# Performance work log

Measured on AMD Instinct MI355X. Metric: run time of the kernel, lower is better.

## Reference

```python
import jax, jax.numpy as jnp
import numpy as np

B, S, D, H, DH, RANK = 1, 2048, 1024, 16, 64, 16
NUM_ITERS = 5
EPS = 1e-6


def setup_inputs() -> dict:
    ks = jax.random.split(jax.random.key(0), 8)
    scale = 1.0 / np.sqrt(D)
    return {
        "x": jax.random.normal(ks[0], (B, S, D), dtype=jnp.float32),
        "Wq": jax.random.normal(ks[1], (D, D), dtype=jnp.float32) * scale,
        "Wk": jax.random.normal(ks[2], (D, D), dtype=jnp.float32) * scale,
        "Wv": jax.random.normal(ks[3], (D, D), dtype=jnp.float32) * scale,
        "Wo": jax.random.normal(ks[4], (D, D), dtype=jnp.float32) * scale,
        "bandwidth": jnp.array(1.0, dtype=jnp.float32),
        "diag_scale": jnp.ones((1, H, 1), dtype=jnp.float32),
        "pos_embedding": jax.random.normal(ks[5], (2048, RANK), dtype=jnp.float32) * 0.02,
        "head_proj": jax.random.normal(ks[6], (H, RANK, RANK), dtype=jnp.float32) * 0.02,
        "reg": jnp.array(0.1, dtype=jnp.float32),
        "lambda_reg": jnp.array(0.1, dtype=jnp.float32),
    }


def reference(x, Wq, Wk, Wv, Wo, bandwidth, diag_scale, pos_embedding, head_proj, reg, lambda_reg):
    b, s, d = x.shape
    h, dh = H, DH

    def heads(t):  # (b,s,d) -> (b,h,s,dh)
        return t.reshape(b, s, h, dh).transpose(0, 2, 1, 3)

    q = heads(x @ Wq)
    k = heads(x @ Wk)
    v = heads(x @ Wv)

    # RBF kernel via norm trick: ||q-k||^2 = ||q||^2 + ||k||^2 - 2 q.k
    bw = jax.nn.softplus(bandwidth) + EPS
    q_nsq = jnp.sum(q * q, axis=-1, keepdims=True)            # (b,h,s,1)
    k_nsq = jnp.sum(k * k, axis=-1, keepdims=True)            # (b,h,s,1)
    dist_sq = q_nsq + jnp.swapaxes(k_nsq, -2, -1) - 2.0 * jnp.einsum('bhsd,bhtd->bhst', q, k)
    dist_sq = jnp.maximum(dist_sq, 0.0)
    K = jnp.exp(-dist_sq / (2.0 * bw * bw))                   # (b,h,s,s)

    lam = jax.nn.softplus(lambda_reg)

    # Preconditioner P = diag(d) + U U^T
    kdiag = jnp.diagonal(K, axis1=-2, axis2=-1)               # (b,h,s)
    diag_p = jax.nn.softplus(kdiag) * diag_scale + reg        # (b,h,s)
    U = jnp.einsum('sr,hrp->hsp', pos_embedding[:s], head_proj)  # (h,s,rank)

    # Preconditioned Richardson iteration for (K + lam I) alpha = V
    alpha = jnp.zeros_like(v)
    for _ in range(NUM_ITERS):
        r = v - (jnp.einsum('bhst,bhtd->bhsd', K, alpha) + lam * alpha)
        ut_r = jnp.einsum('htr,bhtd->bhrd', U, r)
        p = r * diag_p[..., None] + jnp.einsum('hsr,bhrd->bhsd', U, ut_r)
        alpha = alpha + p

    out = jnp.einsum('bhst,bhtd->bhsd', K, alpha)             # output = K alpha
    out = out.transpose(0, 2, 1, 3).reshape(b, s, d) @ Wo
    return out
```

## Files before the change

kernel.cpp:

```cpp
#include <hip/hip_runtime.h>
#include <cstdint>
#include <cstddef>

constexpr int kS  = 2048;
constexpr int kD  = 1024;
constexpr int kH  = 16;
constexpr int kDH = 64;
constexpr int kR  = 16;

typedef __attribute__((ext_vector_type(8))) short bf16x8;
typedef __attribute__((ext_vector_type(4))) float f32x4;

__device__ __forceinline__ unsigned short kar_f2bf(float x) {
  unsigned u = __float_as_uint(x);
  return (unsigned short)((u + 0x7FFFu + ((u >> 16) & 1u)) >> 16);
}
__device__ __forceinline__ float kar_bf2f(short h) {
  return __uint_as_float((unsigned)(unsigned short)h << 16);
}
__device__ __forceinline__ void kar_split_bf(float x, short& hi, short& lo) {
  unsigned short h = kar_f2bf(x);
  float hf = __uint_as_float((unsigned)h << 16);
  hi = (short)h;
  lo = (short)kar_f2bf(x - hf);
}

__global__ __launch_bounds__(64) void kar_scalars_kernel(const float* __restrict__ bw,
                                                         const float* __restrict__ lreg,
                                                         double* __restrict__ SC) {
  if (threadIdx.x == 0) {
    double b = log1p(exp((double)bw[0])) + 1e-6;
    SC[0] = 1.0 / (2.0 * b * b);
    SC[1] = log1p(exp((double)lreg[0]));
  }
}

__global__ __launch_bounds__(256) void kar_u_kernel(const float* __restrict__ pe,
                                                    const float* __restrict__ hp,
                                                    float* __restrict__ U) {
  int o = blockIdx.x * 256 + threadIdx.x;
  int r = o & 15, s = (o >> 4) & 2047, h = o >> 15;
  double acc = 0.0;
#pragma unroll
  for (int rp = 0; rp < kR; rp++)
    acc += (double)pe[s * kR + rp] * (double)hp[((h * kR) + rp) * kR + r];
  U[o] = (float)acc;
}

__global__ __launch_bounds__(256) void kar_utr_partial_kernel(
    const float* __restrict__ Ubuf, const float* __restrict__ rbuf,
    double* __restrict__ utrp) {
  const int h  = blockIdx.y;
  const int sb = blockIdx.x * 128;
  const int t  = threadIdx.x;
  __shared__ float Uch[32][16];
  __shared__ float Rch[32][64];
  double acc[4] = {};
  for (int cs = 0; cs < 128; cs += 32) {
    __syncthreads();
    if (t < 128) {
      const int i = t >> 2, f = (t & 3) * 4;
      *(float4*)&Uch[i][f] = *(const float4*)&Ubuf[((size_t)(h * kS) + sb + cs + i) * kR + f];
    }
#pragma unroll
    for (int rep = 0; rep < 2; rep++) {
      const int e = t + rep * 256;
      const int i = e >> 4, c = (e & 15) * 4;
      *(float4*)&Rch[i][c] = *(const float4*)&rbuf[((size_t)(h * kS) + sb + cs + i) * kDH + c];
    }
    __syncthreads();
    for (int i = 0; i < 32; i++) {
#pragma unroll
      for (int rep = 0; rep < 4; rep++) {
        const int p = t + rep * 256;
        const int r = p >> 6, d = p & 63;
        acc[rep] += (double)Uch[i][r] * (double)Rch[i][d];
      }
    }
  }
#pragma unroll
  for (int rep = 0; rep < 4; rep++) {
    const int p = t + rep * 256;
    const int r = p >> 6, d = p & 63;
    utrp[(((size_t)(h * 16) + blockIdx.x) * kR + r) * kDH + d] = acc[rep];
  }
}

__global__ __launch_bounds__(256) void kar_utr_reduce_kernel(const double* __restrict__ utrp,
                                                             double* __restrict__ utr) {
  int o = blockIdx.x * 256 + threadIdx.x;
  int h = o >> 10, rd = o & 1023;
  double s = 0.0;
#pragma unroll
  for (int j = 0; j < 16; j++) s += utrp[(size_t)h * 16384 + (size_t)j * 1024 + rd];
  utr[o] = s;
}

__global__ __launch_bounds__(256) void kar_update_kernel(
    const float* __restrict__ rsrc, const double* __restrict__ dgp,
    const float* __restrict__ Ubuf, const double* __restrict__ utr,
    float* __restrict__ alpha, int first) {
  int e = blockIdx.x * 256 + threadIdx.x;
  const int d = e & 63;
  const int s = (e >> 6) & 2047;
  const int h = e >> 17;
  const double rv = (double)rsrc[e];
  const double dp = dgp[h * kS + s];
  const float*  Us = &Ubuf[((size_t)(h * kS) + s) * kR];
  const double* uh = &utr[(size_t)h * kR * kDH];
  double sum = 0.0;
#pragma unroll
  for (int ri = 0; ri < kR; ri++) sum += (double)Us[ri] * uh[ri * kDH + d];
  const double p = rv * dp + sum;
  const double an = (first ? 0.0 : (double)alpha[e]) + p;
  alpha[e] = (float)an;
}

__global__ __launch_bounds__(256) void kar_update_t_kernel(
    const float* __restrict__ rsrc, const double* __restrict__ dgp,
    const float* __restrict__ Ubuf, const double* __restrict__ utr,
    float* __restrict__ alpha, short* __restrict__ ath, short* __restrict__ atl,
    int first) {
  const int h = blockIdx.y, s0 = blockIdx.x * 64;
  __shared__ float T[64][65];
  const int t = threadIdx.x;
  const int r16 = t >> 4, c4 = (t & 15) * 4;
  const double* uh = &utr[(size_t)h * kR * kDH];
#pragma unroll
  for (int it = 0; it < 4; it++) {
    const int row = it * 16 + r16;
    const int s = s0 + row;
    const size_t eg = ((size_t)h * kS + s) * kDH + c4;
    const float4 rv4 = *(const float4*)&rsrc[eg];
    const double dp = dgp[h * kS + s];
    const float* Us = &Ubuf[((size_t)h * kS + s) * kR];
    double sum0 = 0.0, sum1 = 0.0, sum2 = 0.0, sum3 = 0.0;
#pragma unroll
    for (int ri = 0; ri < kR; ri++) {
      const double u = (double)Us[ri];
      const double* ur = &uh[ri * kDH + c4];
      sum0 += u * ur[0]; sum1 += u * ur[1];
      sum2 += u * ur[2]; sum3 += u * ur[3];
    }
    double a0 = (first ? 0.0 : (double)alpha[eg + 0]) + ((double)rv4.x * dp + sum0);
    double a1 = (first ? 0.0 : (double)alpha[eg + 1]) + ((double)rv4.y * dp + sum1);
    double a2 = (first ? 0.0 : (double)alpha[eg + 2]) + ((double)rv4.z * dp + sum2);
    double a3 = (first ? 0.0 : (double)alpha[eg + 3]) + ((double)rv4.w * dp + sum3);
    float4 o;
    o.x = (float)a0; o.y = (float)a1; o.z = (float)a2; o.w = (float)a3;
    *(float4*)&alpha[eg] = o;
    T[row][c4] = o.x; T[row][c4 + 1] = o.y; T[row][c4 + 2] = o.z; T[row][c4 + 3] = o.w;
  }
  __syncthreads();
#pragma unroll
  for (int it = 0; it < 4; it++) {
    int d = it * 16 + r16;
    float v0 = T[c4][d], v1 = T[c4 + 1][d], v2 = T[c4 + 2][d], v3 = T[c4 + 3][d];
    short h0, l0, h1, l1, h2, l2, h3, l3;
    kar_split_bf(v0, h0, l0); kar_split_bf(v1, h1, l1);
    kar_split_bf(v2, h2, l2); kar_split_bf(v3, h3, l3);
    *(short4*)&ath[((size_t)h * kDH + d) * kS + s0 + c4] = make_short4(h0, h1, h2, h3);
    *(short4*)&atl[((size_t)h * kDH + d) * kS + s0 + c4] = make_short4(l0, l1, l2, l3);
  }
}


__global__ __launch_bounds__(256) void kar_xsplit_kernel(const float* __restrict__ x,
                                                         short* __restrict__ xh,
                                                         short* __restrict__ xl) {
  size_t e = ((size_t)blockIdx.x * 256 + threadIdx.x) * 4;
  float4 a = *(const float4*)&x[e];
  short h0, l0, h1, l1, h2, l2, h3, l3;
  kar_split_bf(a.x, h0, l0); kar_split_bf(a.y, h1, l1);
  kar_split_bf(a.z, h2, l2); kar_split_bf(a.w, h3, l3);
  *(short4*)&xh[e] = make_short4(h0, h1, h2, h3);
  *(short4*)&xl[e] = make_short4(l0, l1, l2, l3);
}

__global__ __launch_bounds__(256) void kar_wsplit_kernel(
    const float* __restrict__ Wq, const float* __restrict__ Wk,
    const float* __restrict__ Wv, const float* __restrict__ Wo,
    short* __restrict__ WTh, short* __restrict__ WTl) {
  const float* W = (blockIdx.z == 0) ? Wq : (blockIdx.z == 1) ? Wk
                 : (blockIdx.z == 2) ? Wv : Wo;
  short* oh = WTh + (size_t)blockIdx.z * kD * kD;
  short* ol = WTl + (size_t)blockIdx.z * kD * kD;
  const int n0 = blockIdx.x * 64, k0 = blockIdx.y * 64;
  __shared__ float T[64][65];
  const int t = threadIdx.x;
  const int r16 = t >> 4, c4 = (t & 15) * 4;
#pragma unroll
  for (int it = 0; it < 4; it++) {
    int r = it * 16 + r16;
    float4 a = *(const float4*)&W[(size_t)(k0 + r) * kD + n0 + c4];
    T[r][c4] = a.x; T[r][c4 + 1] = a.y; T[r][c4 + 2] = a.z; T[r][c4 + 3] = a.w;
  }
  __syncthreads();
#pragma unroll
  for (int it = 0; it < 4; it++) {
    int n = it * 16 + r16;
    float v0 = T[c4][n], v1 = T[c4 + 1][n], v2 = T[c4 + 2][n], v3 = T[c4 + 3][n];
    short h0, l0, h1, l1, h2, l2, h3, l3;
    kar_split_bf(v0, h0, l0); kar_split_bf(v1, h1, l1);
    kar_split_bf(v2, h2, l2); kar_split_bf(v3, h3, l3);
    *(short4*)&oh[(size_t)(n0 + n) * kD + k0 + c4] = make_short4(h0, h1, h2, h3);
    *(short4*)&ol[(size_t)(n0 + n) * kD + k0 + c4] = make_short4(l0, l1, l2, l3);
  }
}

__global__ __launch_bounds__(256) void kar_mfma_gemm_qkv_kernel(
    const short* __restrict__ xh, const short* __restrict__ xl,
    const short* __restrict__ WTh, const short* __restrict__ WTl,
    float* __restrict__ v,
    short* __restrict__ qsh, short* __restrict__ qsl,
    short* __restrict__ ksh, short* __restrict__ ksl) {
  const int z = blockIdx.z;
  const short* Bh = WTh + (size_t)z * kD * kD;
  const short* Bl = WTl + (size_t)z * kD * kD;
  const int n0 = blockIdx.x * 64;
  const int m0 = blockIdx.y * 128;
  constexpr int LW = 40;
  __shared__ short Xh[128 * LW], Xl[128 * LW], Wh[64 * LW], Wl[64 * LW];
  const int t = threadIdx.x, lane = t & 63, wv = t >> 6;
  const int wm = wv >> 1, wn = wv & 1, l16 = lane & 15, qd = lane >> 4;
  f32x4 acc[4][2];
#pragma unroll
  for (int i = 0; i < 4; i++)
#pragma unroll
    for (int j = 0; j < 2; j++) acc[i][j] = (f32x4){0.f, 0.f, 0.f, 0.f};
  const int xrow = t >> 1, xc = (t & 1) * 16;
  for (int k0 = 0; k0 < kD; k0 += 32) {
    __syncthreads();
    {
      const size_t xs = (size_t)(m0 + xrow) * kD + k0 + xc;
      *(bf16x8*)&Xh[xrow * LW + xc]     = *(const bf16x8*)&xh[xs];
      *(bf16x8*)&Xh[xrow * LW + xc + 8] = *(const bf16x8*)&xh[xs + 8];
      *(bf16x8*)&Xl[xrow * LW + xc]     = *(const bf16x8*)&xl[xs];
      *(bf16x8*)&Xl[xrow * LW + xc + 8] = *(const bf16x8*)&xl[xs + 8];
    }
    if (t < 128) {
      const int wrow = t >> 1, wc = (t & 1) * 16;
      const size_t wsrc = (size_t)(n0 + wrow) * kD + k0 + wc;
      *(bf16x8*)&Wh[wrow * LW + wc]     = *(const bf16x8*)&Bh[wsrc];
      *(bf16x8*)&Wh[wrow * LW + wc + 8] = *(const bf16x8*)&Bh[wsrc + 8];
    } else {
      const int t2 = t - 128, wrow = t2 >> 1, wc = (t2 & 1) * 16;
      const size_t wsrc = (size_t)(n0 + wrow) * kD + k0 + wc;
      *(bf16x8*)&Wl[wrow * LW + wc]     = *(const bf16x8*)&Bl[wsrc];
      *(bf16x8*)&Wl[wrow * LW + wc + 8] = *(const bf16x8*)&Bl[wsrc + 8];
    }
    __syncthreads();
    bf16x8 bH[2], bL[2];
#pragma unroll
    for (int ni = 0; ni < 2; ni++) {
      const int rn = wn * 32 + ni * 16 + l16;
      bH[ni] = *(const bf16x8*)&Wh[rn * LW + qd * 8];
      bL[ni] = *(const bf16x8*)&Wl[rn * LW + qd * 8];
    }
#pragma unroll
    for (int mi = 0; mi < 4; mi++) {
      const int rm = wm * 64 + mi * 16 + l16;
      const bf16x8 aH = *(const bf16x8*)&Xh[rm * LW + qd * 8];
      const bf16x8 aL = *(const bf16x8*)&Xl[rm * LW + qd * 8];
#pragma unroll
      for (int ni = 0; ni < 2; ni++) {
        acc[mi][ni] = __builtin_amdgcn_mfma_f32_16x16x32_bf16(aH, bH[ni], acc[mi][ni], 0, 0, 0);
        acc[mi][ni] = __builtin_amdgcn_mfma_f32_16x16x32_bf16(aL, bH[ni], acc[mi][ni], 0, 0, 0);
        acc[mi][ni] = __builtin_amdgcn_mfma_f32_16x16x32_bf16(aH, bL[ni], acc[mi][ni], 0, 0, 0);
      }
    }
  }
  const int h = blockIdx.x;
#pragma unroll
  for (int mi = 0; mi < 4; mi++)
#pragma unroll
    for (int ni = 0; ni < 2; ni++) {
      const int d = wn * 32 + ni * 16 + l16;
#pragma unroll
      for (int r = 0; r < 4; r++) {
        const int s = m0 + wm * 64 + mi * 16 + qd * 4 + r;
        const float val = acc[mi][ni][r];
        const size_t idx = (((size_t)h * kS) + s) * kDH + d;
        if (z == 2) {
          v[idx] = val;
        } else {
          short hh, ll; kar_split_bf(val, hh, ll);
          if (z == 0) { qsh[idx] = hh; qsl[idx] = ll; }
          else        { ksh[idx] = hh; ksl[idx] = ll; }
        }
      }
    }
}

__global__ __launch_bounds__(256) void kar_mfma_gemm_wo_kernel(
    const short* __restrict__ th, const short* __restrict__ tl,
    const short* __restrict__ Bh, const short* __restrict__ Bl,
    float* __restrict__ outp) {
  const int n0 = blockIdx.x * 64;
  const int m0 = blockIdx.y * 128;
  constexpr int LW = 40;
  __shared__ short Xh[128 * LW], Xl[128 * LW], Wh[64 * LW], Wl[64 * LW];
  const int t = threadIdx.x, lane = t & 63, wv = t >> 6;
  const int wm = wv >> 1, wn = wv & 1, l16 = lane & 15, qd = lane >> 4;
  f32x4 acc[4][2];
#pragma unroll
  for (int i = 0; i < 4; i++)
#pragma unroll
    for (int j = 0; j < 2; j++) acc[i][j] = (f32x4){0.f, 0.f, 0.f, 0.f};
  const int xrow = t >> 1, xc = (t & 1) * 16;
  for (int k0 = 0; k0 < kD; k0 += 32) {
    __syncthreads();
    {
      const size_t xs = (size_t)(m0 + xrow) * kD + k0 + xc;
      *(bf16x8*)&Xh[xrow * LW + xc]     = *(const bf16x8*)&th[xs];
      *(bf16x8*)&Xh[xrow * LW + xc + 8] = *(const bf16x8*)&th[xs + 8];
      *(bf16x8*)&Xl[xrow * LW + xc]     = *(const bf16x8*)&tl[xs];
      *(bf16x8*)&Xl[xrow * LW + xc + 8] = *(const bf16x8*)&tl[xs + 8];
    }
    if (t < 128) {
      const int wrow = t >> 1, wc = (t & 1) * 16;
      const size_t wsrc = (size_t)(n0 + wrow) * kD + k0 + wc;
      *(bf16x8*)&Wh[wrow * LW + wc]     = *(const bf16x8*)&Bh[wsrc];
      *(bf16x8*)&Wh[wrow * LW + wc + 8] = *(const bf16x8*)&Bh[wsrc + 8];
    } else {
      const int t2 = t - 128, wrow = t2 >> 1, wc = (t2 & 1) * 16;
      const size_t wsrc = (size_t)(n0 + wrow) * kD + k0 + wc;
      *(bf16x8*)&Wl[wrow * LW + wc]     = *(const bf16x8*)&Bl[wsrc];
      *(bf16x8*)&Wl[wrow * LW + wc + 8] = *(const bf16x8*)&Bl[wsrc + 8];
    }
    __syncthreads();
    bf16x8 bH[2], bL[2];
#pragma unroll
    for (int ni = 0; ni < 2; ni++) {
      const int rn = wn * 32 + ni * 16 + l16;
      bH[ni] = *(const bf16x8*)&Wh[rn * LW + qd * 8];
      bL[ni] = *(const bf16x8*)&Wl[rn * LW + qd * 8];
    }
#pragma unroll
    for (int mi = 0; mi < 4; mi++) {
      const int rm = wm * 64 + mi * 16 + l16;
      const bf16x8 aH = *(const bf16x8*)&Xh[rm * LW + qd * 8];
      const bf16x8 aL = *(const bf16x8*)&Xl[rm * LW + qd * 8];
#pragma unroll
      for (int ni = 0; ni < 2; ni++) {
        acc[mi][ni] = __builtin_amdgcn_mfma_f32_16x16x32_bf16(aH, bH[ni], acc[mi][ni], 0, 0, 0);
        acc[mi][ni] = __builtin_amdgcn_mfma_f32_16x16x32_bf16(aL, bH[ni], acc[mi][ni], 0, 0, 0);
        acc[mi][ni] = __builtin_amdgcn_mfma_f32_16x16x32_bf16(aH, bL[ni], acc[mi][ni], 0, 0, 0);
      }
    }
  }
#pragma unroll
  for (int mi = 0; mi < 4; mi++)
#pragma unroll
    for (int ni = 0; ni < 2; ni++) {
      const int col = n0 + wn * 32 + ni * 16 + l16;
#pragma unroll
      for (int r = 0; r < 4; r++) {
        const int s = m0 + wm * 64 + mi * 16 + qd * 4 + r;
        outp[(size_t)s * kD + col] = acc[mi][ni][r];
      }
    }
}

__global__ __launch_bounds__(256) void kar_norms2_kernel(
    const short* __restrict__ qsh, const short* __restrict__ qsl,
    const short* __restrict__ ksh, const short* __restrict__ ksl,
    double* __restrict__ qn, double* __restrict__ kn) {
  int o = blockIdx.x * 256 + threadIdx.x;
  const short *sh, *sl; double* dst; int p;
  if (o < kH * kS) { sh = qsh; sl = qsl; dst = qn; p = o; }
  else             { sh = ksh; sl = ksl; dst = kn; p = o - kH * kS; }
  const short* rh = sh + (size_t)p * kDH;
  const short* rl = sl + (size_t)p * kDH;
  double s = 0.0;
  for (int i = 0; i < kDH; i += 4) {
    short4 a = *(const short4*)&rh[i];
    short4 b = *(const short4*)&rl[i];
    double e0 = (double)kar_bf2f(a.x) + (double)kar_bf2f(b.x);
    double e1 = (double)kar_bf2f(a.y) + (double)kar_bf2f(b.y);
    double e2 = (double)kar_bf2f(a.z) + (double)kar_bf2f(b.z);
    double e3 = (double)kar_bf2f(a.w) + (double)kar_bf2f(b.w);
    s += e0 * e0 + e1 * e1 + e2 * e2 + e3 * e3;
  }
  dst[p] = s;
}

__global__ __launch_bounds__(256) void kar_diagp2_kernel(
    const short* __restrict__ qsh, const short* __restrict__ qsl,
    const short* __restrict__ ksh, const short* __restrict__ ksl,
    const double* __restrict__ qn, const double* __restrict__ kn,
    const double* __restrict__ SC, const float* __restrict__ dsc,
    const float* __restrict__ reg, double* __restrict__ dgp) {
  int o = blockIdx.x * 256 + threadIdx.x;
  int h = o >> 11;
  const short* qh = qsh + (size_t)o * kDH;
  const short* ql = qsl + (size_t)o * kDH;
  const short* kh = ksh + (size_t)o * kDH;
  const short* kl = ksl + (size_t)o * kDH;
  double dot = 0.0;
  for (int i = 0; i < kDH; i++) {
    double qi = (double)kar_bf2f(qh[i]) + (double)kar_bf2f(ql[i]);
    double ki = (double)kar_bf2f(kh[i]) + (double)kar_bf2f(kl[i]);
    dot += qi * ki;
  }
  double dist = fmax(qn[o] + kn[o] - 2.0 * dot, 0.0);
  double Kss = exp(-dist * SC[0]);
  double sp  = log1p(exp(Kss));
  dgp[o] = sp * (double)dsc[h] + (double)reg[0];
}

template <bool FINAL>
__global__ __launch_bounds__(256, 2) void kar_mfma_iter4_kernel(
    const short* __restrict__ qsh, const short* __restrict__ qsl,
    const short* __restrict__ ksh, const short* __restrict__ ksl,
    const short* __restrict__ ath, const short* __restrict__ atl,
    const float* __restrict__ alpha, const float* __restrict__ v,
    const double* __restrict__ qn, const double* __restrict__ kn,
    const double* __restrict__ SC, float* __restrict__ outp,
    short* __restrict__ tmph, short* __restrict__ tmpl) {
  constexpr int LDW = 72;
  __shared__ short Kh[64 * LDW], Kl[64 * LDW];
  __shared__ short Ah[64 * LDW], Al[64 * LDW];
  __shared__ short Ph[64 * LDW];
  __shared__ float qns[64];
  const int h   = blockIdx.y;
  const int s0  = blockIdx.x * 64;
  const int tid = threadIdx.x;
  const int lane = tid & 63;
  const int wv   = tid >> 6;
  const int l16  = lane & 15;
  const int qd   = lane >> 4;
  const int row = tid >> 2, c8 = (tid & 3) * 16;
  bf16x8 qH[4][2], qL[4][2];
#pragma unroll
  for (int sq = 0; sq < 4; sq++) {
    const size_t qb = (((size_t)h * kS) + s0 + sq * 16 + l16) * kDH;
    qH[sq][0] = *(const bf16x8*)&qsh[qb + qd * 8];
    qH[sq][1] = *(const bf16x8*)&qsh[qb + 32 + qd * 8];
    qL[sq][0] = *(const bf16x8*)&qsl[qb + qd * 8];
    qL[sq][1] = *(const bf16x8*)&qsl[qb + 32 + qd * 8];
  }
  if (tid < 64) qns[tid] = (float)qn[h * kS + s0 + tid];
  const float cc = (float)SC[0];
  f32x4 acco[4];
#pragma unroll
  for (int i = 0; i < 4; i++) acco[i] = (f32x4){0.f, 0.f, 0.f, 0.f};

  for (int t0 = 0; t0 < kS; t0 += 64) {
    __syncthreads();
    {
      const size_t ksrc = (((size_t)h * kS) + t0 + row) * kDH;
      *(bf16x8*)&Kh[row * LDW + c8]     = *(const bf16x8*)&ksh[ksrc + c8];
      *(bf16x8*)&Kh[row * LDW + c8 + 8] = *(const bf16x8*)&ksh[ksrc + c8 + 8];
      *(bf16x8*)&Kl[row * LDW + c8]     = *(const bf16x8*)&ksl[ksrc + c8];
      *(bf16x8*)&Kl[row * LDW + c8 + 8] = *(const bf16x8*)&ksl[ksrc + c8 + 8];
      const size_t asrc = ((size_t)h * kDH + row) * kS + t0;
      *(bf16x8*)&Ah[row * LDW + c8]     = *(const bf16x8*)&ath[asrc + c8];
      *(bf16x8*)&Ah[row * LDW + c8 + 8] = *(const bf16x8*)&ath[asrc + c8 + 8];
      *(bf16x8*)&Al[row * LDW + c8]     = *(const bf16x8*)&atl[asrc + c8];
      *(bf16x8*)&Al[row * LDW + c8 + 8] = *(const bf16x8*)&atl[asrc + c8 + 8];
    }
    const float knr = (float)kn[h * kS + t0 + wv * 16 + l16];
    __syncthreads();
    f32x4 accp[4];
#pragma unroll
    for (int i = 0; i < 4; i++) accp[i] = (f32x4){0.f, 0.f, 0.f, 0.f};
#pragma unroll
    for (int kt = 0; kt < 2; kt++) {
      const int ko = kt * 32 + qd * 8;
      const bf16x8 bH = *(const bf16x8*)&Kh[(wv * 16 + l16) * LDW + ko];
      const bf16x8 bL = *(const bf16x8*)&Kl[(wv * 16 + l16) * LDW + ko];
#pragma unroll
      for (int sq = 0; sq < 4; sq++) {
        accp[sq] = __builtin_amdgcn_mfma_f32_16x16x32_bf16(qH[sq][kt], bH, accp[sq], 0, 0, 0);
        accp[sq] = __builtin_amdgcn_mfma_f32_16x16x32_bf16(qL[sq][kt], bH, accp[sq], 0, 0, 0);
        accp[sq] = __builtin_amdgcn_mfma_f32_16x16x32_bf16(qH[sq][kt], bL, accp[sq], 0, 0, 0);
      }
    }
#pragma unroll
    for (int sq = 0; sq < 4; sq++) {
#pragma unroll
      for (int r = 0; r < 4; r++) {
        const int srow = sq * 16 + qd * 4 + r;
        const float e2 = fmaf(2.0f, accp[sq][r], -(qns[srow] + knr));
        const float val = __expf(fminf(e2, 0.0f) * cc);
        Ph[srow * LDW + wv * 16 + l16] = (short)kar_f2bf(val);
      }
    }
    __syncthreads();
#pragma unroll
    for (int kt = 0; kt < 2; kt++) {
      const int ko = kt * 32 + qd * 8;
      const bf16x8 bH = *(const bf16x8*)&Ah[(wv * 16 + l16) * LDW + ko];
      const bf16x8 bL = *(const bf16x8*)&Al[(wv * 16 + l16) * LDW + ko];
#pragma unroll
      for (int sq = 0; sq < 4; sq++) {
        const bf16x8 pH = *(const bf16x8*)&Ph[(sq * 16 + l16) * LDW + ko];
        acco[sq] = __builtin_amdgcn_mfma_f32_16x16x32_bf16(pH, bH, acco[sq], 0, 0, 0);
        acco[sq] = __builtin_amdgcn_mfma_f32_16x16x32_bf16(pH, bL, acco[sq], 0, 0, 0);
      }
    }
  }
  const int d = wv * 16 + l16;
  if (FINAL) {
#pragma unroll
    for (int sq = 0; sq < 4; sq++) {
#pragma unroll
      for (int r = 0; r < 4; r++) {
        const int s = s0 + sq * 16 + qd * 4 + r;
        short hh, ll; kar_split_bf(acco[sq][r], hh, ll);
        tmph[(size_t)s * kD + h * kDH + d] = hh;
        tmpl[(size_t)s * kD + h * kDH + d] = ll;
      }
    }
  } else {
    const float lamf = (float)SC[1];
#pragma unroll
    for (int sq = 0; sq < 4; sq++) {
#pragma unroll
      for (int r = 0; r < 4; r++) {
        const int s = s0 + sq * 16 + qd * 4 + r;
        const size_t eg = ((size_t)h * kS + s) * kDH + d;
        outp[eg] = v[eg] - (acco[sq][r] + lamf * alpha[eg]);
      }
    }
  }
}

__global__ __launch_bounds__(256) void kar_gemm_qkv_f32_kernel(
    const float* __restrict__ x,
    const float* __restrict__ Wq, const float* __restrict__ Wk, const float* __restrict__ Wv,
    float* __restrict__ q, float* __restrict__ k, float* __restrict__ v) {
  const float* W = (blockIdx.z == 0) ? Wq : (blockIdx.z == 1) ? Wk : Wv;
  float* outp    = (blockIdx.z == 0) ? q  : (blockIdx.z == 1) ? k  : v;
  const int n0 = blockIdx.x * 64;
  const int m0 = blockIdx.y * 64;
  const int tid = threadIdx.x;
  const int tx = tid & 15, ty = tid >> 4;
  __shared__ float As[16][68];
  __shared__ float Bs[16][68];
  double acc[4][4] = {};
  const int lr = tid >> 2;
  const int lk = (tid & 3) * 4;
  const int br = tid >> 4;
  const int bc = (tid & 15) * 4;
  for (int k0 = 0; k0 < kD; k0 += 16) {
    const float4 a4 = *(const float4*)&x[(size_t)(m0 + lr) * kD + k0 + lk];
    const float4 b4 = *(const float4*)&W[(size_t)(k0 + br) * kD + n0 + bc];
    __syncthreads();
    As[lk + 0][lr] = a4.x; As[lk + 1][lr] = a4.y;
    As[lk + 2][lr] = a4.z; As[lk + 3][lr] = a4.w;
    *(float4*)&Bs[br][bc] = b4;
    __syncthreads();
    float c32[4][4] = {};
#pragma unroll
    for (int kk = 0; kk < 16; kk++) {
      const float4 av = *(const float4*)&As[kk][ty * 4];
      const float4 bv = *(const float4*)&Bs[kk][tx * 4];
      const float a_[4] = {av.x, av.y, av.z, av.w};
      const float b_[4] = {bv.x, bv.y, bv.z, bv.w};
#pragma unroll
      for (int i = 0; i < 4; i++)
#pragma unroll
        for (int j = 0; j < 4; j++) c32[i][j] = fmaf(a_[i], b_[j], c32[i][j]);
    }
#pragma unroll
    for (int i = 0; i < 4; i++)
#pragma unroll
      for (int j = 0; j < 4; j++) acc[i][j] += (double)c32[i][j];
  }
  const int h = n0 >> 6;
#pragma unroll
  for (int i = 0; i < 4; i++) {
    const int s = m0 + ty * 4 + i;
    float4 o;
    o.x = (float)acc[i][0]; o.y = (float)acc[i][1];
    o.z = (float)acc[i][2]; o.w = (float)acc[i][3];
    *(float4*)&outp[((size_t)h * kS + s) * kDH + tx * 4] = o;
  }
}

__global__ __launch_bounds__(256) void kar_gemm_plain_kernel(
    const float* __restrict__ A, const float* __restrict__ W, float* __restrict__ C) {
  const int n0 = blockIdx.x * 64;
  const int m0 = blockIdx.y * 64;
  const int tid = threadIdx.x;
  const int tx = tid & 15, ty = tid >> 4;
  __shared__ float As[16][68];
  __shared__ float Bs[16][68];
  double acc[4][4] = {};
  const int lr = tid >> 2;
  const int lk = (tid & 3) * 4;
  const int br = tid >> 4;
  const int bc = (tid & 15) * 4;
  for (int k0 = 0; k0 < kD; k0 += 16) {
    const float4 a4 = *(const float4*)&A[(size_t)(m0 + lr) * kD + k0 + lk];
    const float4 b4 = *(const float4*)&W[(size_t)(k0 + br) * kD + n0 + bc];
    __syncthreads();
    As[lk + 0][lr] = a4.x; As[lk + 1][lr] = a4.y;
    As[lk + 2][lr] = a4.z; As[lk + 3][lr] = a4.w;
    *(float4*)&Bs[br][bc] = b4;
    __syncthreads();
    float c32[4][4] = {};
#pragma unroll
    for (int kk = 0; kk < 16; kk++) {
      const float4 av = *(const float4*)&As[kk][ty * 4];
      const float4 bv = *(const float4*)&Bs[kk][tx * 4];
      const float a_[4] = {av.x, av.y, av.z, av.w};
      const float b_[4] = {bv.x, bv.y, bv.z, bv.w};
#pragma unroll
      for (int i = 0; i < 4; i++)
#pragma unroll
        for (int j = 0; j < 4; j++) c32[i][j] = fmaf(a_[i], b_[j], c32[i][j]);
    }
#pragma unroll
    for (int i = 0; i < 4; i++)
#pragma unroll
      for (int j = 0; j < 4; j++) acc[i][j] += (double)c32[i][j];
  }
#pragma unroll
  for (int i = 0; i < 4; i++) {
    const int s = m0 + ty * 4 + i;
    float4 o;
    o.x = (float)acc[i][0]; o.y = (float)acc[i][1];
    o.z = (float)acc[i][2]; o.w = (float)acc[i][3];
    *(float4*)&C[(size_t)s * kD + n0 + tx * 4] = o;
  }
}

__global__ __launch_bounds__(256) void kar_norms_f32_kernel(const float* __restrict__ q,
                                                            const float* __restrict__ k,
                                                            double* __restrict__ qn,
                                                            double* __restrict__ kn) {
  int o = blockIdx.x * 256 + threadIdx.x;
  const float* src; double* dst; int p;
  if (o < kH * kS) { src = q; dst = qn; p = o; }
  else             { src = k; dst = kn; p = o - kH * kS; }
  const float* rowp = src + (size_t)p * kDH;
  double s = 0.0;
  for (int i = 0; i < kDH; i += 4) {
    float4 x4 = *(const float4*)&rowp[i];
    s += (double)x4.x * (double)x4.x + (double)x4.y * (double)x4.y +
         (double)x4.z * (double)x4.z + (double)x4.w * (double)x4.w;
  }
  dst[p] = s;
}

__global__ __launch_bounds__(256) void kar_diagp_f32_kernel(
    const float* __restrict__ q, const float* __restrict__ k,
    const double* __restrict__ qn, const double* __restrict__ kn,
    const double* __restrict__ SC, const float* __restrict__ dsc,
    const float* __restrict__ reg, double* __restrict__ dgp) {
  int o = blockIdx.x * 256 + threadIdx.x;
  int h = o >> 11;
  const float* qp = q + (size_t)o * kDH;
  const float* kp = k + (size_t)o * kDH;
  double dot = 0.0;
  for (int i = 0; i < kDH; i++) dot += (double)qp[i] * (double)kp[i];
  double dist = fmax(qn[o] + kn[o] - 2.0 * dot, 0.0);
  double Kss = exp(-dist * SC[0]);
  double sp  = log1p(exp(Kss));
  dgp[o] = sp * (double)dsc[h] + (double)reg[0];
}

template <bool FINAL>
__global__ __launch_bounds__(256, 2) void kar_mfma_iterA_kernel(
    const float* __restrict__ q, const float* __restrict__ k,
    const float* __restrict__ alpha, const float* __restrict__ v,
    const double* __restrict__ qn, const double* __restrict__ kn,
    const double* __restrict__ SC, float* __restrict__ outp) {
  constexpr int LDW = 72;
  __shared__ short Qh[64 * LDW], Ql[64 * LDW];
  __shared__ short Kh[64 * LDW], Kl[64 * LDW];
  __shared__ short Ph[64 * LDW], Pl[64 * LDW];
  __shared__ short Ah[64 * LDW], Al[64 * LDW];
  __shared__ float qns[64], kns[64];
  const int h   = blockIdx.y;
  const int s0  = blockIdx.x * 64;
  const int tid = threadIdx.x;
  const int lane = tid & 63;
  const int wv   = tid >> 6;
  const int l16  = lane & 15;
  const int qd   = lane >> 4;
  const int m16  = wv * 16;
  const float* qh = q + ((size_t)h * kS + s0) * kDH;
  const float* kh = k + (size_t)h * kS * kDH;
  const float* ah = alpha + (size_t)h * kS * kDH;
  {
    const int row = tid >> 4;
    const int c4  = (tid & 15) * 4;
#pragma unroll
    for (int rep = 0; rep < 4; rep++) {
      const int r = rep * 16 + row;
      const float4 a = *(const float4*)&qh[(size_t)r * kDH + c4];
      short h0, l0, h1, l1, h2, l2, h3, l3;
      kar_split_bf(a.x, h0, l0); kar_split_bf(a.y, h1, l1);
      kar_split_bf(a.z, h2, l2); kar_split_bf(a.w, h3, l3);
      *(short4*)&Qh[r * LDW + c4] = make_short4(h0, h1, h2, h3);
      *(short4*)&Ql[r * LDW + c4] = make_short4(l0, l1, l2, l3);
    }
    if (tid < 64) qns[tid] = (float)qn[h * kS + s0 + tid];
  }
  const float cc = (float)SC[0];
  f32x4 acco[4];
#pragma unroll
  for (int i = 0; i < 4; i++) acco[i] = (f32x4){0.f, 0.f, 0.f, 0.f};
  for (int t0 = 0; t0 < kS; t0 += 64) {
    __syncthreads();
    {
      const int row = tid >> 4;
      const int c4  = (tid & 15) * 4;
#pragma unroll
      for (int rep = 0; rep < 4; rep++) {
        const int r = rep * 16 + row;
        const float4 b = *(const float4*)&kh[(size_t)(t0 + r) * kDH + c4];
        short h0, l0, h1, l1, h2, l2, h3, l3;
        kar_split_bf(b.x, h0, l0); kar_split_bf(b.y, h1, l1);
        kar_split_bf(b.z, h2, l2); kar_split_bf(b.w, h3, l3);
        *(short4*)&Kh[r * LDW + c4] = make_short4(h0, h1, h2, h3);
        *(short4*)&Kl[r * LDW + c4] = make_short4(l0, l1, l2, l3);
        const float4 av = *(const float4*)&ah[(size_t)(t0 + r) * kDH + c4];
        kar_split_bf(av.x, h0, l0); kar_split_bf(av.y, h1, l1);
        kar_split_bf(av.z, h2, l2); kar_split_bf(av.w, h3, l3);
        Ah[(c4 + 0) * LDW + r] = h0; Al[(c4 + 0) * LDW + r] = l0;
        Ah[(c4 + 1) * LDW + r] = h1; Al[(c4 + 1) * LDW + r] = l1;
        Ah[(c4 + 2) * LDW + r] = h2; Al[(c4 + 2) * LDW + r] = l2;
        Ah[(c4 + 3) * LDW + r] = h3; Al[(c4 + 3) * LDW + r] = l3;
      }
      if (tid < 64) kns[tid] = (float)kn[h * kS + t0 + tid];
    }
    __syncthreads();
    f32x4 accp[4];
#pragma unroll
    for (int i = 0; i < 4; i++) accp[i] = (f32x4){0.f, 0.f, 0.f, 0.f};
#pragma unroll
    for (int kt = 0; kt < 2; kt++) {
      const int ko = kt * 32 + qd * 8;
      const bf16x8 aH = *(const bf16x8*)&Qh[(m16 + l16) * LDW + ko];
      const bf16x8 aL = *(const bf16x8*)&Ql[(m16 + l16) * LDW + ko];
#pragma unroll
      for (int nt = 0; nt < 4; nt++) {
        const bf16x8 bH = *(const bf16x8*)&Kh[(nt * 16 + l16) * LDW + ko];
        const bf16x8 bL = *(const bf16x8*)&Kl[(nt * 16 + l16) * LDW + ko];
        accp[nt] = __builtin_amdgcn_mfma_f32_16x16x32_bf16(aH, bH, accp[nt], 0, 0, 0);
        accp[nt] = __builtin_amdgcn_mfma_f32_16x16x32_bf16(aL, bH, accp[nt], 0, 0, 0);
        accp[nt] = __builtin_amdgcn_mfma_f32_16x16x32_bf16(aH, bL, accp[nt], 0, 0, 0);
      }
    }
#pragma unroll
    for (int nt = 0; nt < 4; nt++) {
      const int tcol = nt * 16 + l16;
      const float kv = kns[tcol];
#pragma unroll
      for (int r = 0; r < 4; r++) {
        const int srow = m16 + qd * 4 + r;
        const float e2 = fmaf(2.0f, accp[nt][r], -(qns[srow] + kv));
        const float val = __expf(fminf(e2, 0.0f) * cc);
        short hb, lb; kar_split_bf(val, hb, lb);
        Ph[srow * LDW + tcol] = hb;
        Pl[srow * LDW + tcol] = lb;
      }
    }
#pragma unroll
    for (int kt = 0; kt < 2; kt++) {
      const int ko = kt * 32 + qd * 8;
      const bf16x8 pH = *(const bf16x8*)&Ph[(m16 + l16) * LDW + ko];
      const bf16x8 pL = *(const bf16x8*)&Pl[(m16 + l16) * LDW + ko];
#pragma unroll
      for (int dt = 0; dt < 4; dt++) {
        const bf16x8 bH = *(const bf16x8*)&Ah[(dt * 16 + l16) * LDW + ko];
        const bf16x8 bL = *(const bf16x8*)&Al[(dt * 16 + l16) * LDW + ko];
        acco[dt] = __builtin_amdgcn_mfma_f32_16x16x32_bf16(pH, bH, acco[dt], 0, 0, 0);
        acco[dt] = __builtin_amdgcn_mfma_f32_16x16x32_bf16(pL, bH, acco[dt], 0, 0, 0);
        acco[dt] = __builtin_amdgcn_mfma_f32_16x16x32_bf16(pH, bL, acco[dt], 0, 0, 0);
      }
    }
  }
  if (FINAL) {
#pragma unroll
    for (int dt = 0; dt < 4; dt++) {
#pragma unroll
      for (int r = 0; r < 4; r++) {
        const int s = s0 + m16 + qd * 4 + r;
        const int d = dt * 16 + l16;
        outp[(size_t)s * kD + h * kDH + d] = acco[dt][r];
      }
    }
  } else {
    const float lamf = (float)SC[1];
#pragma unroll
    for (int dt = 0; dt < 4; dt++) {
#pragma unroll
      for (int r = 0; r < 4; r++) {
        const int s = s0 + m16 + qd * 4 + r;
        const int d = dt * 16 + l16;
        const size_t eg = ((size_t)h * kS + s) * kDH + d;
        outp[eg] = v[eg] - (acco[dt][r] + lamf * alpha[eg]);
      }
    }
  }
}

extern "C" void kernel_launch(void* const* d_in, const int* in_sizes, int n_in,
                              void* d_out, int out_size, void* d_ws, size_t ws_size,
                              hipStream_t stream) {
  (void)in_sizes; (void)n_in; (void)out_size;
  const float* x    = (const float*)d_in[0];
  const float* Wq   = (const float*)d_in[1];
  const float* Wk   = (const float*)d_in[2];
  const float* Wv   = (const float*)d_in[3];
  const float* Wo   = (const float*)d_in[4];
  const float* bw   = (const float*)d_in[5];
  const float* dsc  = (const float*)d_in[6];
  const float* pe   = (const float*)d_in[7];
  const float* hp   = (const float*)d_in[8];
  const float* reg  = (const float*)d_in[9];
  const float* lreg = (const float*)d_in[10];
  float* out = (float*)d_out;

  char* w = (char*)d_ws;
  size_t off = 0;
  auto take = [&](size_t bytes) -> void* {
    void* p = w + off;
    off += (bytes + 255) & ~(size_t)255;
    return p;
  };
  const size_t HSD = (size_t)kH * kS * kDH;

  float*  v_    = (float*)take(HSD * 4);
  float*  alpha = (float*)take(HSD * 4);
  float*  rbuf  = (float*)take(HSD * 4);
  short*  qsh   = (short*)take(HSD * 2);
  short*  qsl   = (short*)take(HSD * 2);
  short*  ksh   = (short*)take(HSD * 2);
  short*  ksl   = (short*)take(HSD * 2);
  short*  ath   = (short*)take(HSD * 2);
  short*  atl   = (short*)take(HSD * 2);
  short*  xh    = (short*)take((size_t)kS * kD * 2);
  short*  xl    = (short*)take((size_t)kS * kD * 2);
  short*  WTh   = (short*)take((size_t)4 * kD * kD * 2);
  short*  WTl   = (short*)take((size_t)4 * kD * kD * 2);
  double* qn    = (double*)take((size_t)kH * kS * 8);
  double* kn    = (double*)take((size_t)kH * kS * 8);
  double* dgp   = (double*)take((size_t)kH * kS * 8);
  float*  U     = (float*)take((size_t)kH * kS * kR * 4);
  double* utr   = (double*)take((size_t)kH * kR * kDH * 8);
  double* utrp  = (double*)take((size_t)kH * 16 * kR * kDH * 8);
  double* SC    = (double*)take(256);
  const size_t need_new = off;

  if (ws_size >= need_new) {
    kar_scalars_kernel<<<1, 64, 0, stream>>>(bw, lreg, SC);
    kar_xsplit_kernel<<<2048, 256, 0, stream>>>(x, xh, xl);
    kar_wsplit_kernel<<<dim3(16, 16, 4), 256, 0, stream>>>(Wq, Wk, Wv, Wo, WTh, WTl);
    kar_mfma_gemm_qkv_kernel<<<dim3(16, 16, 3), 256, 0, stream>>>(
        xh, xl, WTh, WTl, v_, qsh, qsl, ksh, ksl);
    kar_norms2_kernel<<<256, 256, 0, stream>>>(qsh, qsl, ksh, ksl, qn, kn);
    kar_u_kernel<<<2048, 256, 0, stream>>>(pe, hp, U);
    kar_diagp2_kernel<<<128, 256, 0, stream>>>(qsh, qsl, ksh, ksl, qn, kn, SC, dsc, reg, dgp);

    kar_utr_partial_kernel<<<dim3(16, kH), 256, 0, stream>>>(U, v_, utrp);
    kar_utr_reduce_kernel<<<64, 256, 0, stream>>>(utrp, utr);
    kar_update_t_kernel<<<dim3(32, kH), 256, 0, stream>>>(v_, dgp, U, utr, alpha, ath, atl, 1);

    for (int it = 1; it < 5; it++) {
      kar_mfma_iter4_kernel<false><<<dim3(32, kH), 256, 0, stream>>>(
          qsh, qsl, ksh, ksl, ath, atl, alpha, v_, qn, kn, SC, rbuf, nullptr, nullptr);
      kar_utr_partial_kernel<<<dim3(16, kH), 256, 0, stream>>>(U, rbuf, utrp);
      kar_utr_reduce_kernel<<<64, 256, 0, stream>>>(utrp, utr);
      kar_update_t_kernel<<<dim3(32, kH), 256, 0, stream>>>(rbuf, dgp, U, utr, alpha, ath, atl, 0);
    }

    kar_mfma_iter4_kernel<true><<<dim3(32, kH), 256, 0, stream>>>(
        qsh, qsl, ksh, ksl, ath, atl, alpha, v_, qn, kn, SC, rbuf, xh, xl);
    kar_mfma_gemm_wo_kernel<<<dim3(16, 16), 256, 0, stream>>>(
        xh, xl, WTh + (size_t)3 * kD * kD, WTl + (size_t)3 * kD * kD, out);
  } else {
    size_t off2 = 0;
    auto take2 = [&](size_t bytes) -> void* {
      void* p = w + off2;
      off2 += (bytes + 255) & ~(size_t)255;
      return p;
    };
    float*  q2    = (float*)take2(HSD * 4);
    float*  k2    = (float*)take2(HSD * 4);
    float*  v2    = (float*)take2(HSD * 4);
    float*  al2   = (float*)take2(HSD * 4);
    float*  rb2   = (float*)take2(HSD * 4);
    float*  tmp2  = (float*)take2((size_t)kS * kD * 4);
    double* qn2   = (double*)take2((size_t)kH * kS * 8);
    double* kn2   = (double*)take2((size_t)kH * kS * 8);
    double* dgp2  = (double*)take2((size_t)kH * kS * 8);
    float*  U2    = (float*)take2((size_t)kH * kS * kR * 4);
    double* utr2  = (double*)take2((size_t)kH * kR * kDH * 8);
    double* utrp2 = (double*)take2((size_t)kH * 16 * kR * kDH * 8);
    double* SC2   = (double*)take2(256);

    kar_scalars_kernel<<<1, 64, 0, stream>>>(bw, lreg, SC2);
    kar_gemm_qkv_f32_kernel<<<dim3(16, 32, 3), 256, 0, stream>>>(x, Wq, Wk, Wv, q2, k2, v2);
    kar_norms_f32_kernel<<<256, 256, 0, stream>>>(q2, k2, qn2, kn2);
    kar_u_kernel<<<2048, 256, 0, stream>>>(pe, hp, U2);
    kar_diagp_f32_kernel<<<128, 256, 0, stream>>>(q2, k2, qn2, kn2, SC2, dsc, reg, dgp2);

    kar_utr_partial_kernel<<<dim3(16, kH), 256, 0, stream>>>(U2, v2, utrp2);
    kar_utr_reduce_kernel<<<64, 256, 0, stream>>>(utrp2, utr2);
    kar_update_kernel<<<8192, 256, 0, stream>>>(v2, dgp2, U2, utr2, al2, 1);

    for (int it = 1; it < 5; it++) {
      kar_mfma_iterA_kernel<false><<<dim3(32, kH), 256, 0, stream>>>(
          q2, k2, al2, v2, qn2, kn2, SC2, rb2);
      kar_utr_partial_kernel<<<dim3(16, kH), 256, 0, stream>>>(U2, rb2, utrp2);
      kar_utr_reduce_kernel<<<64, 256, 0, stream>>>(utrp2, utr2);
      kar_update_kernel<<<8192, 256, 0, stream>>>(rb2, dgp2, U2, utr2, al2, 0);
    }
    kar_mfma_iterA_kernel<true><<<dim3(32, kH), 256, 0, stream>>>(
        q2, k2, al2, v2, qn2, kn2, SC2, tmp2);
    kar_gemm_plain_kernel<<<dim3(16, 32), 256, 0, stream>>>(tmp2, Wo, out);
  }
}
```

Baseline: 693.5 us.

## Fuse U^T r partial reduction into residual kernel and drop alpha low bf16 part

The residual kernel now computes the per-block U^T r partial sums in its epilogue, so the separate utr_partial launch inside the iteration loop is gone. The partial buffer is resized to 32 blocks per head to match. Alpha is also kept only as a single bf16 (hi) part, which halves the MFMA count and LDS/global traffic for the K*alpha product. The cost is lower precision in K*alpha, which could hurt accuracy of the Richardson iteration.

```diff
diff --git a/kernel.cpp b/kernel.cpp
--- a/kernel.cpp
+++ b/kernel.cpp
@@ -51,12 +51,12 @@
     const float* __restrict__ Ubuf, const float* __restrict__ rbuf,
     double* __restrict__ utrp) {
   const int h  = blockIdx.y;
-  const int sb = blockIdx.x * 128;
+  const int sb = blockIdx.x * 64;
   const int t  = threadIdx.x;
   __shared__ float Uch[32][16];
   __shared__ float Rch[32][64];
   double acc[4] = {};
-  for (int cs = 0; cs < 128; cs += 32) {
+  for (int cs = 0; cs < 64; cs += 32) {
     __syncthreads();
     if (t < 128) {
       const int i = t >> 2, f = (t & 3) * 4;
@@ -82,7 +82,7 @@
   for (int rep = 0; rep < 4; rep++) {
     const int p = t + rep * 256;
     const int r = p >> 6, d = p & 63;
-    utrp[(((size_t)(h * 16) + blockIdx.x) * kR + r) * kDH + d] = acc[rep];
+    utrp[(((size_t)(h * 32) + blockIdx.x) * kR + r) * kDH + d] = acc[rep];
   }
 }
 
@@ -92,7 +92,7 @@
   int h = o >> 10, rd = o & 1023;
   double s = 0.0;
 #pragma unroll
-  for (int j = 0; j < 16; j++) s += utrp[(size_t)h * 16384 + (size_t)j * 1024 + rd];
+  for (int j = 0; j < 32; j++) s += utrp[(size_t)h * 32768 + (size_t)j * 1024 + rd];
   utr[o] = s;
 }
 
@@ -119,8 +119,7 @@
 __global__ __launch_bounds__(256) void kar_update_t_kernel(
     const float* __restrict__ rsrc, const double* __restrict__ dgp,
     const float* __restrict__ Ubuf, const double* __restrict__ utr,
-    float* __restrict__ alpha, short* __restrict__ ath, short* __restrict__ atl,
-    int first) {
+    float* __restrict__ alpha, short* __restrict__ ath, int first) {
   const int h = blockIdx.y, s0 = blockIdx.x * 64;
   __shared__ float T[64][65];
   const int t = threadIdx.x;
@@ -156,11 +155,9 @@
   for (int it = 0; it < 4; it++) {
     int d = it * 16 + r16;
     float v0 = T[c4][d], v1 = T[c4 + 1][d], v2 = T[c4 + 2][d], v3 = T[c4 + 3][d];
-    short h0, l0, h1, l1, h2, l2, h3, l3;
-    kar_split_bf(v0, h0, l0); kar_split_bf(v1, h1, l1);
-    kar_split_bf(v2, h2, l2); kar_split_bf(v3, h3, l3);
-    *(short4*)&ath[((size_t)h * kDH + d) * kS + s0 + c4] = make_short4(h0, h1, h2, h3);
-    *(short4*)&atl[((size_t)h * kDH + d) * kS + s0 + c4] = make_short4(l0, l1, l2, l3);
+    *(short4*)&ath[((size_t)h * kDH + d) * kS + s0 + c4] =
+        make_short4((short)kar_f2bf(v0), (short)kar_f2bf(v1),
+                    (short)kar_f2bf(v2), (short)kar_f2bf(v3));
   }
 }
 
@@ -410,19 +407,21 @@
 }
 
 template <bool FINAL>
-__global__ __launch_bounds__(256, 2) void kar_mfma_iter4_kernel(
+__global__ __launch_bounds__(256, 2) void kar_mfma_iter5_kernel(
     const short* __restrict__ qsh, const short* __restrict__ qsl,
     const short* __restrict__ ksh, const short* __restrict__ ksl,
-    const short* __restrict__ ath, const short* __restrict__ atl,
+    const short* __restrict__ ath,
     const float* __restrict__ alpha, const float* __restrict__ v,
     const double* __restrict__ qn, const double* __restrict__ kn,
     const double* __restrict__ SC, float* __restrict__ outp,
-    short* __restrict__ tmph, short* __restrict__ tmpl) {
+    short* __restrict__ tmph, short* __restrict__ tmpl,
+    const float* __restrict__ Ug, double* __restrict__ utrp) {
   constexpr int LDW = 72;
   __shared__ short Kh[64 * LDW], Kl[64 * LDW];
-  __shared__ short Ah[64 * LDW], Al[64 * LDW];
+  __shared__ short Ah[64 * LDW];
   __shared__ short Ph[64 * LDW];
   __shared__ float qns[64];
+  __shared__ float Ub[64][16];
   const int h   = blockIdx.y;
   const int s0  = blockIdx.x * 64;
   const int tid = threadIdx.x;
@@ -457,8 +456,6 @@
       const size_t asrc = ((size_t)h * kDH + row) * kS + t0;
       *(bf16x8*)&Ah[row * LDW + c8]     = *(const bf16x8*)&ath[asrc + c8];
       *(bf16x8*)&Ah[row * LDW + c8 + 8] = *(const bf16x8*)&ath[asrc + c8 + 8];
-      *(bf16x8*)&Al[row * LDW + c8]     = *(const bf16x8*)&atl[asrc + c8];
-      *(bf16x8*)&Al[row * LDW + c8 + 8] = *(const bf16x8*)&atl[asrc + c8 + 8];
     }
     const float knr = (float)kn[h * kS + t0 + wv * 16 + l16];
     __syncthreads();
@@ -492,12 +489,10 @@
     for (int kt = 0; kt < 2; kt++) {
       const int ko = kt * 32 + qd * 8;
       const bf16x8 bH = *(const bf16x8*)&Ah[(wv * 16 + l16) * LDW + ko];
-      const bf16x8 bL = *(const bf16x8*)&Al[(wv * 16 + l16) * LDW + ko];
 #pragma unroll
       for (int sq = 0; sq < 4; sq++) {
         const bf16x8 pH = *(const bf16x8*)&Ph[(sq * 16 + l16) * LDW + ko];
         acco[sq] = __builtin_amdgcn_mfma_f32_16x16x32_bf16(pH, bH, acco[sq], 0, 0, 0);
-        acco[sq] = __builtin_amdgcn_mfma_f32_16x16x32_bf16(pH, bL, acco[sq], 0, 0, 0);
       }
     }
   }
@@ -515,14 +510,53 @@
     }
   } else {
     const float lamf = (float)SC[1];
+    float rv[4][4];
 #pragma unroll
     for (int sq = 0; sq < 4; sq++) {
 #pragma unroll
       for (int r = 0; r < 4; r++) {
         const int s = s0 + sq * 16 + qd * 4 + r;
         const size_t eg = ((size_t)h * kS + s) * kDH + d;
-        outp[eg] = v[eg] - (acco[sq][r] + lamf * alpha[eg]);
-      }
+        const float rr = v[eg] - (acco[sq][r] + lamf * alpha[eg]);
+        rv[sq][r] = rr;
+        outp[eg] = rr;
+      }
+    }
+    *(float4*)&Ub[tid >> 2][(tid & 3) * 4] =
+        *(const float4*)&Ug[((size_t)h * kS + s0 + (tid >> 2)) * kR + (tid & 3) * 4];
+    __syncthreads();
+    double uacc[16];
+#pragma unroll
+    for (int ri = 0; ri < 16; ri++) uacc[ri] = 0.0;
+#pragma unroll
+    for (int sq = 0; sq < 4; sq++) {
+#pragma unroll
+      for (int r = 0; r < 4; r++) {
+        const int sl = sq * 16 + qd * 4 + r;
+        const double rval = (double)rv[sq][r];
+        const float4 u0 = *(const float4*)&Ub[sl][0];
+        const float4 u1 = *(const float4*)&Ub[sl][4];
+        const float4 u2 = *(const float4*)&Ub[sl][8];
+        const float4 u3 = *(const float4*)&Ub[sl][12];
+        uacc[0]  += (double)u0.x * rval; uacc[1]  += (double)u0.y * rval;
+        uacc[2]  += (double)u0.z * rval; uacc[3]  += (double)u0.w * rval;
+        uacc[4]  += (double)u1.x * rval; uacc[5]  += (double)u1.y * rval;
+        uacc[6]  += (double)u1.z * rval; uacc[7]  += (double)u1.w * rval;
+        uacc[8]  += (double)u2.x * rval; uacc[9]  += (double)u2.y * rval;
+        uacc[10] += (double)u2.z * rval; uacc[11] += (double)u2.w * rval;
+        uacc[12] += (double)u3.x * rval; uacc[13] += (double)u3.y * rval;
+        uacc[14] += (double)u3.z * rval; uacc[15] += (double)u3.w * rval;
+      }
+    }
+#pragma unroll
+    for (int ri = 0; ri < 16; ri++) {
+      uacc[ri] += __shfl_xor(uacc[ri], 16, 64);
+      uacc[ri] += __shfl_xor(uacc[ri], 32, 64);
+    }
+    if (qd == 0) {
+#pragma unroll
+      for (int ri = 0; ri < 16; ri++)
+        utrp[(((size_t)(h * 32) + blockIdx.x) * kR + ri) * kDH + d] = uacc[ri];
     }
   }
 }
@@ -835,7 +869,6 @@
   short*  ksh   = (short*)take(HSD * 2);
   short*  ksl   = (short*)take(HSD * 2);
   short*  ath   = (short*)take(HSD * 2);
-  short*  atl   = (short*)take(HSD * 2);
   short*  xh    = (short*)take((size_t)kS * kD * 2);
   short*  xl    = (short*)take((size_t)kS * kD * 2);
   short*  WTh   = (short*)take((size_t)4 * kD * kD * 2);
@@ -845,7 +878,7 @@
   double* dgp   = (double*)take((size_t)kH * kS * 8);
   float*  U     = (float*)take((size_t)kH * kS * kR * 4);
   double* utr   = (double*)take((size_t)kH * kR * kDH * 8);
-  double* utrp  = (double*)take((size_t)kH * 16 * kR * kDH * 8);
+  double* utrp  = (double*)take((size_t)kH * 32 * kR * kDH * 8);
   double* SC    = (double*)take(256);
   const size_t need_new = off;
 
@@ -859,20 +892,19 @@
     kar_u_kernel<<<2048, 256, 0, stream>>>(pe, hp, U);
     kar_diagp2_kernel<<<128, 256, 0, stream>>>(qsh, qsl, ksh, ksl, qn, kn, SC, dsc, reg, dgp);
 
-    kar_utr_partial_kernel<<<dim3(16, kH), 256, 0, stream>>>(U, v_, utrp);
+    kar_utr_partial_kernel<<<dim3(32, kH), 256, 0, stream>>>(U, v_, utrp);
     kar_utr_reduce_kernel<<<64, 256, 0, stream>>>(utrp, utr);
-    kar_update_t_kernel<<<dim3(32, kH), 256, 0, stream>>>(v_, dgp, U, utr, alpha, ath, atl, 1);
+    kar_update_t_kernel<<<dim3(32, kH), 256, 0, stream>>>(v_, dgp, U, utr, alpha, ath, 1);
 
     for (int it = 1; it < 5; it++) {
-      kar_mfma_iter4_kernel<false><<<dim3(32, kH), 256, 0, stream>>>(
-          qsh, qsl, ksh, ksl, ath, atl, alpha, v_, qn, kn, SC, rbuf, nullptr, nullptr);
-      kar_utr_partial_kernel<<<dim3(16, kH), 256, 0, stream>>>(U, rbuf, utrp);
+      kar_mfma_iter5_kernel<false><<<dim3(32, kH), 256, 0, stream>>>(
+          qsh, qsl, ksh, ksl, ath, alpha, v_, qn, kn, SC, rbuf, nullptr, nullptr, U, utrp);
       kar_utr_reduce_kernel<<<64, 256, 0, stream>>>(utrp, utr);
-      kar_update_t_kernel<<<dim3(32, kH), 256, 0, stream>>>(rbuf, dgp, U, utr, alpha, ath, atl, 0);
-    }
-
-    kar_mfma_iter4_kernel<true><<<dim3(32, kH), 256, 0, stream>>>(
-        qsh, qsl, ksh, ksl, ath, atl, alpha, v_, qn, kn, SC, rbuf, xh, xl);
+      kar_update_t_kernel<<<dim3(32, kH), 256, 0, stream>>>(rbuf, dgp, U, utr, alpha, ath, 0);
+    }
+
+    kar_mfma_iter5_kernel<true><<<dim3(32, kH), 256, 0, stream>>>(
+        qsh, qsl, ksh, ksl, ath, alpha, v_, qn, kn, SC, rbuf, xh, xl, U, utrp);
     kar_mfma_gemm_wo_kernel<<<dim3(16, 16), 256, 0, stream>>>(
         xh, xl, WTh + (size_t)3 * kD * kD, WTl + (size_t)3 * kD * kD, out);
   } else {
@@ -893,7 +925,7 @@
     double* dgp2  = (double*)take2((size_t)kH * kS * 8);
     float*  U2    = (float*)take2((size_t)kH * kS * kR * 4);
     double* utr2  = (double*)take2((size_t)kH * kR * kDH * 8);
-    double* utrp2 = (double*)take2((size_t)kH * 16 * kR * kDH * 8);
+    double* utrp2 = (double*)take2((size_t)kH * 32 * kR * kDH * 8);
     double* SC2   = (double*)take2(256);
 
     kar_scalars_kernel<<<1, 64, 0, stream>>>(bw, lreg, SC2);
@@ -902,14 +934,14 @@
     kar_u_kernel<<<2048, 256, 0, stream>>>(pe, hp, U2);
     kar_diagp_f32_kernel<<<128, 256, 0, stream>>>(q2, k2, qn2, kn2, SC2, dsc, reg, dgp2);
 
-    kar_utr_partial_kernel<<<dim3(16, kH), 256, 0, stream>>>(U2, v2, utrp2);
+    kar_utr_partial_kernel<<<dim3(32, kH), 256, 0, stream>>>(U2, v2, utrp2);
     kar_utr_reduce_kernel<<<64, 256, 0, stream>>>(utrp2, utr2);
     kar_update_kernel<<<8192, 256, 0, stream>>>(v2, dgp2, U2, utr2, al2, 1);
 
     for (int it = 1; it < 5; it++) {
       kar_mfma_iterA_kernel<false><<<dim3(32, kH), 256, 0, stream>>>(
           q2, k2, al2, v2, qn2, kn2, SC2, rb2);
-      kar_utr_partial_kernel<<<dim3(16, kH), 256, 0, stream>>>(U2, rb2, utrp2);
+      kar_utr_partial_kernel<<<dim3(32, kH), 256, 0, stream>>>(U2, rb2, utrp2);
       kar_utr_reduce_kernel<<<64, 256, 0, stream>>>(utrp2, utr2);
       kar_update_kernel<<<8192, 256, 0, stream>>>(rb2, dgp2, U2, utr2, al2, 0);
     }
```

Result: faster. 612.6 us (-11.7%).
